# Optimization experiments

Measured on AMD Instinct MI355X. Metric: run time of the kernel, lower is better.

Reference implementation:

```python
import jax, jax.numpy as jnp
import numpy as np

H = 1024   # hidden_size
E = 6      # num_experts
LS = 4     # sparse (MoE) layers
LD = 4     # dense layers
CAP = 4    # expert capacity: max(min(1, int(1*1.25/6)), MIN_EXPERT_CAPACITY=4)
LOSS_COEF = 0.01
SECOND_THRESHOLD = 0.2
EPS = 1e-9


def _bn(x, g, b):
    # BatchNorm1d, training-style batch statistics (biased variance), eps=1e-5
    mu = x.mean(0)
    var = ((x - mu) ** 2).mean(0)
    return g * (x - mu) * jax.lax.rsqrt(var + 1e-5) + b


def _top2_gating(x, wg, key):
    # x: (b, n=1, d) -> dispatch/combine (b, n, e, cap), scalar aux loss
    dt = x.dtype
    raw = jax.nn.softmax(jnp.einsum('bnd,de->bne', x, wg), axis=-1)
    idx1 = jnp.argmax(raw, -1)
    m1 = jax.nn.one_hot(idx1, E, dtype=dt)
    g1 = jnp.sum(raw * m1, -1)
    wo1 = raw * (1.0 - m1)
    idx2 = jnp.argmax(wo1, -1)
    m2 = jax.nn.one_hot(idx2, E, dtype=dt)
    g2 = jnp.sum(wo1 * m2, -1)
    den = g1 + g2 + EPS
    g1, g2 = g1 / den, g2 / den
    # load-balancing loss
    loss = jnp.mean(raw.mean(-2) * m1.mean(-2)) * (E * E)
    # 'random' second-expert policy
    probs = jax.random.uniform(key, g2.shape, dtype=dt)
    m2 = m2 * (probs < (g2 / SECOND_THRESHOLD)).astype(dt)[..., None]
    # positions in capacity buffer (exclusive cumsum over token dim)
    p1 = (jnp.cumsum(m1, axis=1) - m1) * m1
    m1 = m1 * (p1 < CAP).astype(dt)
    m1_cnt = m1.sum(axis=1, keepdims=True)
    m1_flat = m1.sum(-1)
    p1 = p1.sum(-1)
    g1 = g1 * m1_flat
    p2 = ((jnp.cumsum(m2, axis=1) - m2) + m1_cnt) * m2
    m2 = m2 * (p2 < CAP).astype(dt)
    m2_flat = m2.sum(-1)
    p2 = p2.sum(-1)
    g2 = g2 * m2_flat
    ohc1 = jax.nn.one_hot(p1.astype(jnp.int32), CAP, dtype=dt)
    ohc2 = jax.nn.one_hot(p2.astype(jnp.int32), CAP, dtype=dt)
    combine = ((g1 * m1_flat)[..., None, None]
               * jax.nn.one_hot(idx1, E, dtype=dt)[..., None] * ohc1[..., None, :]
               + (g2 * m2_flat)[..., None, None]
               * jax.nn.one_hot(idx2, E, dtype=dt)[..., None] * ohc2[..., None, :])
    dispatch = (combine != 0).astype(dt)
    return dispatch, combine, loss


def _moe_layer(x, W, b, g, be, wg, w1, key):
    x = x @ W + b                      # Linear
    raw = x
    x3 = x[:, None, :]                 # SqueezeLayer: (b, 1, d)
    dispatch, combine, loss = _top2_gating(x3, wg, key)
    ei = jnp.einsum('bnd,bnec->ebcd', x3, dispatch)   # (E, b, CAP, d)
    e, bb, c, d = ei.shape
    eo = jax.nn.relu(jnp.einsum('end,edh->enh', ei.reshape(e, bb * c, d), w1))
    out = jnp.einsum('ebcd,bnec->bnd', eo.reshape(e, bb, c, d), combine)[:, 0, :]
    x = raw + out                      # residual
    x = jax.nn.relu(_bn(x, g, be))     # dropout inactive (eval)
    return x, LOSS_COEF * loss


def setup_inputs() -> dict:
    key = jax.random.key(0)
    ks = jax.random.split(key, 8)
    B, IN, OUT = 2048, 2048, 256
    sc = lambda f: 1.0 / np.sqrt(f)
    f32 = jnp.float32
    return {
        'x': jax.random.normal(ks[0], (B, IN), f32),
        'in_W': jax.random.normal(ks[1], (IN, H), f32) * sc(IN),
        'in_b': jnp.zeros((H,), f32),
        'in_g': jnp.ones((H,), f32),
        'in_be': jnp.zeros((H,), f32),
        'sp_W': jax.random.normal(ks[2], (LS, H, H), f32) * sc(H),
        'sp_b': jnp.zeros((LS, H), f32),
        'sp_g': jnp.ones((LS, H), f32),
        'sp_be': jnp.zeros((LS, H), f32),
        'sp_gate': jax.random.normal(ks[3], (LS, H, E), f32) * sc(H),
        'sp_w1': jax.random.normal(ks[4], (LS, E, H, H), f32) * sc(H),
        'dn_W': jax.random.normal(ks[5], (LD, H, H), f32) * sc(H),
        'dn_b': jnp.zeros((LD, H), f32),
        'dn_g': jnp.ones((LD, H), f32),
        'dn_be': jnp.zeros((LD, H), f32),
        'out_W': jax.random.normal(ks[6], (H, OUT), f32) * sc(H),
        'out_b': jnp.zeros((OUT,), f32),
    }


def reference(x, in_W, in_b, in_g, in_be, sp_W, sp_b, sp_g, sp_be, sp_gate, sp_w1,
              dn_W, dn_b, dn_g, dn_be, out_W, out_b):
    h = jax.nn.relu(_bn(x @ in_W + in_b, in_g, in_be))  # input layer (dropout eval)
    loss = jnp.zeros((), h.dtype)
    base = jax.random.key(42)
    for i in range(LS):
        h, l = _moe_layer(h, sp_W[i], sp_b[i], sp_g[i], sp_be[i],
                          sp_gate[i], sp_w1[i], jax.random.fold_in(base, i))
        loss = loss + l
    for i in range(LD):
        h = jax.nn.relu(_bn(h @ dn_W[i] + dn_b[i], dn_g[i], dn_be[i]))
    return h @ out_W + out_b, loss
```

## Files before the change

kernel.cpp:

```cpp
#include <hip/hip_runtime.h>

typedef unsigned int uint;
typedef unsigned short ushort;
typedef short bf16x8 __attribute__((ext_vector_type(8)));
typedef ushort ushort4v __attribute__((ext_vector_type(4)));
typedef float f32x4 __attribute__((ext_vector_type(4)));

#define HD 1024
#define BT 2048
#define NEXP 6
#define MAXR 4096
#define GT 16

typedef __attribute__((address_space(1))) void as1_void;
typedef __attribute__((address_space(3))) void as3_void;
#define ASYNC16(g, l) \
  __builtin_amdgcn_global_load_lds((as1_void*)(const void*)(g), (as3_void*)(void*)(l), 16, 0, 0)

__device__ static inline ushort f32_to_bf16(float f) {
  uint u = __float_as_uint(f);
  u = (u + 0x7fffu + ((u >> 16) & 1u)) >> 16;
  return (ushort)u;
}
__device__ static inline float bf16_to_f32(ushort h) {
  return __uint_as_float(((uint)h) << 16);
}
__device__ static inline void split2(float f, ushort* hi, ushort* lo) {
  ushort h = f32_to_bf16(f);
  *hi = h;
  *lo = f32_to_bf16(f - bf16_to_f32(h));
}

__host__ __device__ static inline unsigned rotl32(unsigned v, int n) {
  return (v << n) | (v >> (32 - n));
}
__host__ __device__ static inline void tf2x32(unsigned k0, unsigned k1,
                                              unsigned x0, unsigned x1,
                                              unsigned* o0, unsigned* o1) {
  unsigned ks0 = k0, ks1 = k1, ks2 = k0 ^ k1 ^ 0x1BD11BDAu;
  x0 += ks0; x1 += ks1;
  const int ra[4] = {13, 15, 26, 6};
  const int rb[4] = {17, 29, 16, 24};
  #pragma unroll
  for (int r = 0; r < 4; ++r) { x0 += x1; x1 = rotl32(x1, ra[r]); x1 ^= x0; }
  x0 += ks1; x1 += ks2 + 1u;
  #pragma unroll
  for (int r = 0; r < 4; ++r) { x0 += x1; x1 = rotl32(x1, rb[r]); x1 ^= x0; }
  x0 += ks2; x1 += ks0 + 2u;
  #pragma unroll
  for (int r = 0; r < 4; ++r) { x0 += x1; x1 = rotl32(x1, ra[r]); x1 ^= x0; }
  x0 += ks0; x1 += ks1 + 3u;
  #pragma unroll
  for (int r = 0; r < 4; ++r) { x0 += x1; x1 = rotl32(x1, rb[r]); x1 ^= x0; }
  x0 += ks1; x1 += ks2 + 4u;
  #pragma unroll
  for (int r = 0; r < 4; ++r) { x0 += x1; x1 = rotl32(x1, ra[r]); x1 ^= x0; }
  x0 += ks2; x1 += ks0 + 5u;
  *o0 = x0; *o1 = x1;
}

__global__ void init_ws_k(int* cnt, float* loss) {
  int t = threadIdx.x;
  if (t < 32) cnt[t] = 0;
  if (t == 32) loss[0] = 0.0f;
}

__global__ __launch_bounds__(256) void transpose_split_k(
    const float* __restrict__ W, ushort* __restrict__ Th, ushort* __restrict__ Tl,
    int K, int N) {
  size_t boff = (size_t)blockIdx.z * K * N;
  W += boff; Th += boff; Tl += boff;
  __shared__ float T[32][33];
  int n0 = blockIdx.x * 32, k0 = blockIdx.y * 32;
  int tid = threadIdx.x;
  int r = tid >> 3, c4 = (tid & 7) * 4;
  float4 v = *(const float4*)&W[(size_t)(k0 + r) * N + n0 + c4];
  T[c4 + 0][r] = v.x; T[c4 + 1][r] = v.y; T[c4 + 2][r] = v.z; T[c4 + 3][r] = v.w;
  __syncthreads();
  ushort4v hh, ll;
  #pragma unroll
  for (int j = 0; j < 4; ++j) {
    float f = T[r][c4 + j];
    ushort h, l; split2(f, &h, &l);
    hh[j] = h; ll[j] = l;
  }
  size_t o = (size_t)(n0 + r) * K + k0 + c4;
  *(ushort4v*)&Th[o] = hh;
  *(ushort4v*)&Tl[o] = ll;
}

__global__ __launch_bounds__(256) void split_plain_k(
    const float* __restrict__ X, ushort* __restrict__ Xh, ushort* __restrict__ Xl) {
  size_t i = ((size_t)blockIdx.x * 256 + threadIdx.x) * 4;
  float4 v = *(const float4*)&X[i];
  ushort4v hh, ll;
  float f[4] = {v.x, v.y, v.z, v.w};
  #pragma unroll
  for (int j = 0; j < 4; ++j) { ushort h, l; split2(f[j], &h, &l); hh[j] = h; ll[j] = l; }
  *(ushort4v*)&Xh[i] = hh;
  *(ushort4v*)&Xl[i] = ll;
}

template <int MODE>
__global__ __launch_bounds__(512, 4) void gemm_mfma_k(
    const ushort* __restrict__ Ah, const ushort* __restrict__ Al,
    const ushort* __restrict__ Bh, const ushort* __restrict__ Bl,
    float* __restrict__ P,
    const int* __restrict__ cnt, const int* __restrict__ list,
    int N, int K, int ksteps) {
  int bz = blockIdx.z;
  int row0 = blockIdx.y * 128, col0 = blockIdx.x * 128;
  int nrows = 0, kbase = 0;
  if (MODE == 2) {
    size_t wo = (size_t)bz * N * K;
    Bh += wo; Bl += wo;
    nrows = cnt[bz];
    list += bz * MAXR;
    if (row0 >= nrows) return;
  } else {
    P += (size_t)bz * BT * N;
    kbase = bz * ksteps * 32;
  }
  __shared__ ushort sAh[2][4096], sAl[2][4096], sBh[2][4096], sBl[2][4096];
  int tid = threadIdx.x;
  int lane = tid & 63, w = tid >> 6;
  int wm = (w & 3) * 32, wn = (w >> 2) * 64;

  const ushort *pAh, *pAl, *pBh, *pBl;
  {
    int ci = tid;
    int r = ci >> 2;
    int cl = (ci & 3) ^ ((r ^ (r >> 2)) & 3);
    int ra = row0 + r;
    if (MODE == 2) ra = (ra < nrows) ? (list[ra] & (BT - 1)) : 0;
    size_t ao = (size_t)ra * K + kbase + cl * 8;
    size_t bo = (size_t)(col0 + r) * K + kbase + cl * 8;
    pAh = Ah + ao; pAl = Al + ao;
    pBh = Bh + bo; pBl = Bl + bo;
  }
  int lb = w * 512;

  int fr = lane & 15, cq = lane >> 4;
  int offA[2], offB[4];
  #pragma unroll
  for (int i = 0; i < 2; ++i) {
    int rA = wm + i * 16 + fr;
    offA[i] = rA * 32 + (cq ^ ((rA ^ (rA >> 2)) & 3)) * 8;
  }
  #pragma unroll
  for (int i = 0; i < 4; ++i) {
    int rB = wn + i * 16 + fr;
    offB[i] = rB * 32 + (cq ^ ((rB ^ (rB >> 2)) & 3)) * 8;
  }

  f32x4 acc[2][4] = {};

#define STAGE(buf, ko)                    \
  do {                                    \
    ASYNC16(pAh + (ko), sAh[buf] + lb);   \
    ASYNC16(pAl + (ko), sAl[buf] + lb);   \
    ASYNC16(pBh + (ko), sBh[buf] + lb);   \
    ASYNC16(pBl + (ko), sBl[buf] + lb);   \
  } while (0)

  STAGE(0, 0);
  __syncthreads();

  int cur = 0;
  for (int ks = 0; ks < ksteps; ++ks) {
    if (ks + 1 < ksteps) STAGE(cur ^ 1, (ks + 1) * 32);

    bf16x8 ah[2], al[2], bh[4], bl[4];
    #pragma unroll
    for (int i = 0; i < 2; ++i) {
      ah[i] = *(const bf16x8*)&sAh[cur][offA[i]];
      al[i] = *(const bf16x8*)&sAl[cur][offA[i]];
    }
    #pragma unroll
    for (int i = 0; i < 4; ++i) {
      bh[i] = *(const bf16x8*)&sBh[cur][offB[i]];
      bl[i] = *(const bf16x8*)&sBl[cur][offB[i]];
    }
    __builtin_amdgcn_s_setprio(1);
    #pragma unroll
    for (int mi = 0; mi < 2; ++mi)
      #pragma unroll
      for (int ni = 0; ni < 4; ++ni) {
        acc[mi][ni] = __builtin_amdgcn_mfma_f32_16x16x32_bf16(ah[mi], bh[ni], acc[mi][ni], 0, 0, 0);
        acc[mi][ni] = __builtin_amdgcn_mfma_f32_16x16x32_bf16(ah[mi], bl[ni], acc[mi][ni], 0, 0, 0);
        acc[mi][ni] = __builtin_amdgcn_mfma_f32_16x16x32_bf16(al[mi], bh[ni], acc[mi][ni], 0, 0, 0);
      }
    __builtin_amdgcn_s_setprio(0);
    __syncthreads();
    cur ^= 1;
  }
#undef STAGE

  if (MODE == 2) {
    #pragma unroll
    for (int mi = 0; mi < 2; ++mi) {
      int rb = row0 + wm + mi * 16 + cq * 4;
      #pragma unroll
      for (int r = 0; r < 4; ++r) {
        int row = rb + r;
        if (row < nrows) {
          size_t dro = (size_t)list[row] * N;
          #pragma unroll
          for (int ni = 0; ni < 4; ++ni)
            P[dro + col0 + wn + ni * 16 + fr] = fmaxf(acc[mi][ni][r], 0.0f);
        }
      }
    }
  } else {
    #pragma unroll
    for (int mi = 0; mi < 2; ++mi) {
      int rb = row0 + wm + mi * 16 + cq * 4;
      #pragma unroll
      for (int r = 0; r < 4; ++r) {
        size_t ro = (size_t)(rb + r) * N;
        #pragma unroll
        for (int ni = 0; ni < 4; ++ni)
          P[ro + col0 + wn + ni * 16 + fr] = acc[mi][ni][r];
      }
    }
  }
}

template <int NS>
__global__ __launch_bounds__(256) void reduce_dense_k(
    const float* __restrict__ P, const float* __restrict__ bias,
    float* __restrict__ xl, float* __restrict__ psum) {
  int c = blockIdx.x * 256 + threadIdx.x;
  int r0 = blockIdx.y * 64;
  float bv = bias[c];
  float s = 0.0f;
  for (int r = r0; r < r0 + 64; ++r) {
    float v = bv;
    #pragma unroll
    for (int j = 0; j < NS; ++j) v += P[(size_t)j * BT * HD + (size_t)r * HD + c];
    xl[(size_t)r * HD + c] = v;
    s += v;
  }
  psum[blockIdx.y * HD + c] = s;
}

template <int NS>
__global__ __launch_bounds__(256) void reduce_split_k(
    const float* __restrict__ P, const float* __restrict__ bias,
    float* __restrict__ xl, ushort* __restrict__ Xh, ushort* __restrict__ Xl2) {
  int c = blockIdx.x * 256 + threadIdx.x;
  int r0 = blockIdx.y * 64;
  float bv = bias[c];
  for (int r = r0; r < r0 + 64; ++r) {
    float v = bv;
    #pragma unroll
    for (int j = 0; j < NS; ++j) v += P[(size_t)j * BT * HD + (size_t)r * HD + c];
    xl[(size_t)r * HD + c] = v;
    ushort h, l; split2(v, &h, &l);
    Xh[(size_t)r * HD + c] = h;
    Xl2[(size_t)r * HD + c] = l;
  }
}

__global__ __launch_bounds__(256) void reduce_out_k(
    const float* __restrict__ P, const float* __restrict__ bias,
    float* __restrict__ out) {
  int c = threadIdx.x;
  int r0 = blockIdx.y * 64;
  float bv = bias[c];
  for (int r = r0; r < r0 + 64; ++r) {
    float v = bv;
    #pragma unroll
    for (int j = 0; j < 8; ++j) v += P[(size_t)j * BT * 256 + (size_t)r * 256 + c];
    out[(size_t)r * 256 + c] = v;
  }
}

__global__ __launch_bounds__(256) void gating_k(
    const float* __restrict__ xl, const float* __restrict__ wg,
    int* __restrict__ cnt, int* __restrict__ toklist,
    float* __restrict__ g1o, float* __restrict__ g2o,
    float* __restrict__ loss, unsigned key0, unsigned key1) {
  int tid = threadIdx.x;
  int lane = tid & 63, wv = tid >> 6;
  int q = lane >> 4, ql = lane & 15;
  int t = wv * 4 + q;
  int b = blockIdx.x * GT + t;

  const float* row = xl + (size_t)b * HD;
  float p[NEXP] = {0, 0, 0, 0, 0, 0};
  for (int d = ql; d < HD; d += 16) {
    float xv = row[d];
    const float* w = wg + (size_t)d * NEXP;
    #pragma unroll
    for (int e = 0; e < NEXP; ++e) p[e] += xv * w[e];
  }
  #pragma unroll
  for (int off = 8; off > 0; off >>= 1)
    #pragma unroll
    for (int e = 0; e < NEXP; ++e) p[e] += __shfl_xor(p[e], off);

  __shared__ int   li1[GT], li2[GT];
  __shared__ float lg1[GT], lg2[GT], lgg1[GT];
  __shared__ int   base_s[NEXP];

  if (ql == 0) {
    float mx = p[0];
    #pragma unroll
    for (int e = 1; e < NEXP; ++e) mx = fmaxf(mx, p[e]);
    float ex[NEXP], s = 0.0f;
    #pragma unroll
    for (int e = 0; e < NEXP; ++e) { ex[e] = expf(p[e] - mx); s += ex[e]; }
    float raw[NEXP];
    #pragma unroll
    for (int e = 0; e < NEXP; ++e) raw[e] = ex[e] / s;
    int i1 = 0; float gg1 = raw[0];
    #pragma unroll
    for (int e = 1; e < NEXP; ++e) if (raw[e] > gg1) { gg1 = raw[e]; i1 = e; }
    int i2 = -1; float gg2 = -1.0f;
    #pragma unroll
    for (int e = 0; e < NEXP; ++e) {
      float v = (e == i1) ? 0.0f : raw[e];
      if (v > gg2) { gg2 = v; i2 = e; }
    }
    float den = gg1 + gg2 + 1e-9f;
    float g1n = gg1 / den;
    float g2n = gg2 / den;
    unsigned o0, o1;
    tf2x32(key0, key1, 0u, (unsigned)b, &o0, &o1);
    unsigned bits = o0 ^ o1;
    float prob = __uint_as_float((bits >> 9) | 0x3f800000u) - 1.0f;
    int keep = prob < (g2n / 0.2f);
    li1[t] = i1;
    li2[t] = keep ? i2 : -1;
    lg1[t] = g1n;
    lg2[t] = keep ? g2n : 0.0f;
    lgg1[t] = gg1;
  }
  __syncthreads();

  if (tid < NEXP) {
    int c = 0;
    for (int j = 0; j < GT; ++j) c += (li1[j] == tid) + (li2[j] == tid);
    base_s[tid] = (c > 0) ? atomicAdd(&cnt[tid], c) : 0;
  }
  if (tid == 64) {
    float s = 0.0f;
    for (int j = 0; j < GT; ++j) s += lgg1[j];
    atomicAdd(loss, s);
  }
  __syncthreads();

  if (tid < GT) {
    int tt = tid;
    int i1 = li1[tt], i2 = li2[tt];
    int bb = blockIdx.x * GT + tt;
    g1o[bb] = lg1[tt];
    g2o[bb] = lg2[tt];
    int o1 = 0, o2 = 0;
    for (int j = 0; j < tt; ++j) {
      o1 += (li1[j] == i1) + (li2[j] == i1);
      o2 += (li1[j] == i2) + (li2[j] == i2);
    }
    toklist[i1 * MAXR + base_s[i1] + o1] = bb;
    if (i2 >= 0) toklist[i2 * MAXR + base_s[i2] + o2] = BT + bb;
  }
}

__global__ __launch_bounds__(256) void combine_sum_k(
    const float* __restrict__ xl, const float* __restrict__ eo,
    const float* __restrict__ g1o, const float* __restrict__ g2o,
    float* __restrict__ y, float* __restrict__ psum) {
  int c = blockIdx.x * 256 + threadIdx.x;
  int r0 = blockIdx.y * 64;
  float s = 0.0f;
  for (int r = r0; r < r0 + 64; ++r) {
    float v = xl[(size_t)r * HD + c];
    float w1g = g1o[r];
    v += w1g * eo[(size_t)r * HD + c];
    float w2g = g2o[r];
    if (w2g != 0.0f) v += w2g * eo[(size_t)(r + BT) * HD + c];
    y[(size_t)r * HD + c] = v;
    s += v;
  }
  psum[blockIdx.y * HD + c] = s;
}

__global__ __launch_bounds__(256) void var_partial_k(
    const float* __restrict__ src, const float* __restrict__ psum,
    float* __restrict__ psumsq) {
  int c = blockIdx.x * 256 + threadIdx.x;
  float s = 0.0f;
  #pragma unroll
  for (int i = 0; i < 32; ++i) s += psum[i * HD + c];
  float mu = s * (1.0f / 2048.0f);
  int r0 = blockIdx.y * 64;
  float ss = 0.0f;
  for (int r = r0; r < r0 + 64; ++r) {
    float d = src[(size_t)r * HD + c] - mu;
    ss += d * d;
  }
  psumsq[blockIdx.y * HD + c] = ss;
}

__global__ __launch_bounds__(256) void bn_split_k(
    const float* __restrict__ src, const float* __restrict__ psum,
    const float* __restrict__ psumsq, const float* __restrict__ gamma,
    const float* __restrict__ beta, ushort* __restrict__ Hh,
    ushort* __restrict__ Hl) {
  int c = blockIdx.x * 256 + threadIdx.x;
  float s = 0.0f, ss = 0.0f;
  #pragma unroll
  for (int i = 0; i < 32; ++i) { s += psum[i * HD + c]; ss += psumsq[i * HD + c]; }
  float mu = s * (1.0f / 2048.0f);
  float var = ss * (1.0f / 2048.0f);
  float inv = 1.0f / sqrtf(var + 1e-5f);
  float ga = gamma[c], be = beta[c];
  int r0 = blockIdx.y * 64;
  for (int r = r0; r < r0 + 64; ++r) {
    float v = src[(size_t)r * HD + c];
    float o = fmaxf(ga * (v - mu) * inv + be, 0.0f);
    ushort h, l; split2(o, &h, &l);
    Hh[(size_t)r * HD + c] = h;
    Hl[(size_t)r * HD + c] = l;
  }
}

__global__ void finalize_loss_k(const float* __restrict__ loss, float* __restrict__ out) {
  if (threadIdx.x == 0) out[BT * 256] = loss[0] * (0.01f * 36.0f / 12288.0f);
}

extern "C" void kernel_launch(void* const* d_in, const int* in_sizes, int n_in,
                              void* d_out, int out_size, void* d_ws, size_t ws_size,
                              hipStream_t stream) {
  const float* x     = (const float*)d_in[0];
  const float* in_W  = (const float*)d_in[1];
  const float* in_b  = (const float*)d_in[2];
  const float* in_g  = (const float*)d_in[3];
  const float* in_be = (const float*)d_in[4];
  const float* sp_W  = (const float*)d_in[5];
  const float* sp_b  = (const float*)d_in[6];
  const float* sp_g  = (const float*)d_in[7];
  const float* sp_be = (const float*)d_in[8];
  const float* sp_gate = (const float*)d_in[9];
  const float* sp_w1 = (const float*)d_in[10];
  const float* dn_W  = (const float*)d_in[11];
  const float* dn_b  = (const float*)d_in[12];
  const float* dn_g  = (const float*)d_in[13];
  const float* dn_be = (const float*)d_in[14];
  const float* out_W = (const float*)d_in[15];
  const float* out_b = (const float*)d_in[16];
  float* out = (float*)d_out;

  char* base = (char*)d_ws;
  size_t off = 0;
  auto alloc = [&](size_t bytes) { void* p = base + off; off = (off + bytes + 255) & ~(size_t)255; return p; };
  float*  xl     = (float*)alloc((size_t)BT * HD * 4);
  float*  P      = (float*)alloc((size_t)4 * BT * HD * 4);
  float*  eo     = P;
  float*  y      = P + (size_t)4 * 1024 * 1024;
  float*  psum   = (float*)alloc(32 * HD * 4);
  float*  psumsq = (float*)alloc(32 * HD * 4);
  float*  g1o    = (float*)alloc(BT * 4);
  float*  g2o    = (float*)alloc(BT * 4);
  float*  loss   = (float*)alloc(256);
  int*    cnt    = (int*)alloc(256);
  int*    toklist= (int*)alloc(NEXP * MAXR * 4);
  ushort* Hh     = (ushort*)alloc((size_t)BT * HD * 2);
  ushort* Hl     = (ushort*)alloc((size_t)BT * HD * 2);
  ushort* XLh    = (ushort*)alloc((size_t)BT * HD * 2);
  ushort* XLl    = (ushort*)alloc((size_t)BT * HD * 2);
  ushort* inWTh  = (ushort*)alloc((size_t)2048 * HD * 2);
  ushort* inWTl  = (ushort*)alloc((size_t)2048 * HD * 2);
  ushort* spWTh  = (ushort*)alloc((size_t)4 * HD * HD * 2);
  ushort* spWTl  = (ushort*)alloc((size_t)4 * HD * HD * 2);
  ushort* dnWTh  = (ushort*)alloc((size_t)4 * HD * HD * 2);
  ushort* dnWTl  = (ushort*)alloc((size_t)4 * HD * HD * 2);
  ushort* outWTh = (ushort*)alloc((size_t)HD * 256 * 2);
  ushort* outWTl = (ushort*)alloc((size_t)HD * 256 * 2);
  ushort* w1Th   = (ushort*)alloc((size_t)24 * HD * HD * 2);
  ushort* w1Tl   = (ushort*)alloc((size_t)24 * HD * HD * 2);
  ushort* Xh     = w1Th;
  ushort* Xl     = w1Th + (size_t)BT * 2048;

  unsigned lk0[4], lk1[4];
  for (int i = 0; i < 4; ++i) tf2x32(0u, 42u, 0u, (unsigned)i, &lk0[i], &lk1[i]);

  dim3 blk(256);
  dim3 gblk(512);
  init_ws_k<<<1, 64, 0, stream>>>(cnt, loss);

  transpose_split_k<<<dim3(32, 64, 1), blk, 0, stream>>>(in_W, inWTh, inWTl, 2048, HD);
  transpose_split_k<<<dim3(32, 32, 4), blk, 0, stream>>>(sp_W, spWTh, spWTl, HD, HD);
  transpose_split_k<<<dim3(32, 32, 4), blk, 0, stream>>>(dn_W, dnWTh, dnWTl, HD, HD);
  transpose_split_k<<<dim3(8, 32, 1), blk, 0, stream>>>(out_W, outWTh, outWTl, HD, 256);
  split_plain_k<<<(BT * 2048) / 1024, blk, 0, stream>>>(x, Xh, Xl);

  gemm_mfma_k<0><<<dim3(8, 16, 4), gblk, 0, stream>>>(Xh, Xl, inWTh, inWTl, P,
                                                      nullptr, nullptr, HD, 2048, 16);
  reduce_dense_k<4><<<dim3(4, 32), blk, 0, stream>>>(P, in_b, xl, psum);
  transpose_split_k<<<dim3(32, 32, 24), blk, 0, stream>>>(sp_w1, w1Th, w1Tl, HD, HD);
  var_partial_k<<<dim3(4, 32), blk, 0, stream>>>(xl, psum, psumsq);
  bn_split_k<<<dim3(4, 32), blk, 0, stream>>>(xl, psum, psumsq, in_g, in_be, Hh, Hl);

  for (int i = 0; i < 4; ++i) {
    gemm_mfma_k<0><<<dim3(8, 16, 4), gblk, 0, stream>>>(Hh, Hl, spWTh + (size_t)i * HD * HD,
                                                        spWTl + (size_t)i * HD * HD, P,
                                                        nullptr, nullptr, HD, HD, 8);
    reduce_split_k<4><<<dim3(4, 32), blk, 0, stream>>>(P, sp_b + i * HD, xl, XLh, XLl);
    gating_k<<<BT / GT, blk, 0, stream>>>(xl, sp_gate + (size_t)i * HD * NEXP,
                                          cnt + i * 8, toklist, g1o, g2o, loss, lk0[i], lk1[i]);
    gemm_mfma_k<2><<<dim3(8, 32, NEXP), gblk, 0, stream>>>(XLh, XLl,
                                                           w1Th + (size_t)i * NEXP * HD * HD,
                                                           w1Tl + (size_t)i * NEXP * HD * HD,
                                                           eo, cnt + i * 8, toklist, HD, HD, 32);
    combine_sum_k<<<dim3(4, 32), blk, 0, stream>>>(xl, eo, g1o, g2o, y, psum);
    var_partial_k<<<dim3(4, 32), blk, 0, stream>>>(y, psum, psumsq);
    bn_split_k<<<dim3(4, 32), blk, 0, stream>>>(y, psum, psumsq, sp_g + i * HD,
                                                sp_be + i * HD, Hh, Hl);
  }

  for (int i = 0; i < 4; ++i) {
    gemm_mfma_k<0><<<dim3(8, 16, 4), gblk, 0, stream>>>(Hh, Hl, dnWTh + (size_t)i * HD * HD,
                                                        dnWTl + (size_t)i * HD * HD, P,
                                                        nullptr, nullptr, HD, HD, 8);
    reduce_dense_k<4><<<dim3(4, 32), blk, 0, stream>>>(P, dn_b + i * HD, xl, psum);
    var_partial_k<<<dim3(4, 32), blk, 0, stream>>>(xl, psum, psumsq);
    bn_split_k<<<dim3(4, 32), blk, 0, stream>>>(xl, psum, psumsq, dn_g + i * HD,
                                                dn_be + i * HD, Hh, Hl);
  }

  gemm_mfma_k<0><<<dim3(2, 16, 8), gblk, 0, stream>>>(Hh, Hl, outWTh, outWTl, P,
                                                      nullptr, nullptr, 256, HD, 4);
  reduce_out_k<<<dim3(1, 32), blk, 0, stream>>>(P, out_b, out);
  finalize_loss_k<<<1, 64, 0, stream>>>(loss, out);
}
```

Baseline: 1.147 ms.

## Narrow GEMM tiles to 128x64 and widen reduction grids with separate BN fold kernels

```diff
diff --git a/kernel.cpp b/kernel.cpp
--- a/kernel.cpp
+++ b/kernel.cpp
@@ -11,6 +11,8 @@
 #define NEXP 6
 #define MAXR 4096
 #define GT 16
+#define NG 128
+#define RG 16
 
 typedef __attribute__((address_space(1))) void as1_void;
 typedef __attribute__((address_space(3))) void as3_void;
@@ -102,14 +104,14 @@
 }
 
 template <int MODE>
-__global__ __launch_bounds__(512, 4) void gemm_mfma_k(
+__global__ __launch_bounds__(512, 6) void gemm_mfma_k(
     const ushort* __restrict__ Ah, const ushort* __restrict__ Al,
     const ushort* __restrict__ Bh, const ushort* __restrict__ Bl,
     float* __restrict__ P,
     const int* __restrict__ cnt, const int* __restrict__ list,
     int N, int K, int ksteps) {
   int bz = blockIdx.z;
-  int row0 = blockIdx.y * 128, col0 = blockIdx.x * 128;
+  int row0 = blockIdx.y * 128, col0 = blockIdx.x * 64;
   int nrows = 0, kbase = 0;
   if (MODE == 2) {
     size_t wo = (size_t)bz * N * K;
@@ -121,46 +123,49 @@
     P += (size_t)bz * BT * N;
     kbase = bz * ksteps * 32;
   }
-  __shared__ ushort sAh[2][4096], sAl[2][4096], sBh[2][4096], sBl[2][4096];
+  __shared__ ushort sAh[2][4096], sAl[2][4096], sBh[2][2048], sBl[2][2048];
   int tid = threadIdx.x;
   int lane = tid & 63, w = tid >> 6;
-  int wm = (w & 3) * 32, wn = (w >> 2) * 64;
-
-  const ushort *pAh, *pAl, *pBh, *pBl;
+  int wm = (w & 3) * 32;
+  int wn = (w >> 2) * 32;
+
+  const ushort *pAh, *pAl, *pBh = Bh, *pBl = Bl;
   {
-    int ci = tid;
-    int r = ci >> 2;
-    int cl = (ci & 3) ^ ((r ^ (r >> 2)) & 3);
+    int r = tid >> 2;
+    int cl = (tid & 3) ^ ((r ^ (r >> 2)) & 3);
     int ra = row0 + r;
     if (MODE == 2) ra = (ra < nrows) ? (list[ra] & (BT - 1)) : 0;
     size_t ao = (size_t)ra * K + kbase + cl * 8;
+    pAh = Ah + ao; pAl = Al + ao;
+  }
+  if (tid < 256) {
+    int r = tid >> 2;
+    int cl = (tid & 3) ^ ((r ^ (r >> 2)) & 3);
     size_t bo = (size_t)(col0 + r) * K + kbase + cl * 8;
-    pAh = Ah + ao; pAl = Al + ao;
     pBh = Bh + bo; pBl = Bl + bo;
   }
   int lb = w * 512;
 
   int fr = lane & 15, cq = lane >> 4;
-  int offA[2], offB[4];
+  int offA[2], offB[2];
   #pragma unroll
   for (int i = 0; i < 2; ++i) {
     int rA = wm + i * 16 + fr;
     offA[i] = rA * 32 + (cq ^ ((rA ^ (rA >> 2)) & 3)) * 8;
-  }
-  #pragma unroll
-  for (int i = 0; i < 4; ++i) {
     int rB = wn + i * 16 + fr;
     offB[i] = rB * 32 + (cq ^ ((rB ^ (rB >> 2)) & 3)) * 8;
   }
 
-  f32x4 acc[2][4] = {};
-
-#define STAGE(buf, ko)                    \
-  do {                                    \
-    ASYNC16(pAh + (ko), sAh[buf] + lb);   \
-    ASYNC16(pAl + (ko), sAl[buf] + lb);   \
-    ASYNC16(pBh + (ko), sBh[buf] + lb);   \
-    ASYNC16(pBl + (ko), sBl[buf] + lb);   \
+  f32x4 acc[2][2] = {};
+
+#define STAGE(buf, ko)                       \
+  do {                                       \
+    ASYNC16(pAh + (ko), sAh[buf] + lb);      \
+    ASYNC16(pAl + (ko), sAl[buf] + lb);      \
+    if (w < 4) {                             \
+      ASYNC16(pBh + (ko), sBh[buf] + lb);    \
+      ASYNC16(pBl + (ko), sBl[buf] + lb);    \
+    }                                        \
   } while (0)
 
   STAGE(0, 0);
@@ -170,14 +175,11 @@
   for (int ks = 0; ks < ksteps; ++ks) {
     if (ks + 1 < ksteps) STAGE(cur ^ 1, (ks + 1) * 32);
 
-    bf16x8 ah[2], al[2], bh[4], bl[4];
+    bf16x8 ah[2], al[2], bh[2], bl[2];
     #pragma unroll
     for (int i = 0; i < 2; ++i) {
       ah[i] = *(const bf16x8*)&sAh[cur][offA[i]];
       al[i] = *(const bf16x8*)&sAl[cur][offA[i]];
-    }
-    #pragma unroll
-    for (int i = 0; i < 4; ++i) {
       bh[i] = *(const bf16x8*)&sBh[cur][offB[i]];
       bl[i] = *(const bf16x8*)&sBl[cur][offB[i]];
     }
@@ -185,7 +187,7 @@
     #pragma unroll
     for (int mi = 0; mi < 2; ++mi)
       #pragma unroll
-      for (int ni = 0; ni < 4; ++ni) {
+      for (int ni = 0; ni < 2; ++ni) {
         acc[mi][ni] = __builtin_amdgcn_mfma_f32_16x16x32_bf16(ah[mi], bh[ni], acc[mi][ni], 0, 0, 0);
         acc[mi][ni] = __builtin_amdgcn_mfma_f32_16x16x32_bf16(ah[mi], bl[ni], acc[mi][ni], 0, 0, 0);
         acc[mi][ni] = __builtin_amdgcn_mfma_f32_16x16x32_bf16(al[mi], bh[ni], acc[mi][ni], 0, 0, 0);
@@ -206,7 +208,7 @@
         if (row < nrows) {
           size_t dro = (size_t)list[row] * N;
           #pragma unroll
-          for (int ni = 0; ni < 4; ++ni)
+          for (int ni = 0; ni < 2; ++ni)
             P[dro + col0 + wn + ni * 16 + fr] = fmaxf(acc[mi][ni][r], 0.0f);
         }
       }
@@ -219,7 +221,7 @@
       for (int r = 0; r < 4; ++r) {
         size_t ro = (size_t)(rb + r) * N;
         #pragma unroll
-        for (int ni = 0; ni < 4; ++ni)
+        for (int ni = 0; ni < 2; ++ni)
           P[ro + col0 + wn + ni * 16 + fr] = acc[mi][ni][r];
       }
     }
@@ -231,10 +233,10 @@
     const float* __restrict__ P, const float* __restrict__ bias,
     float* __restrict__ xl, float* __restrict__ psum) {
   int c = blockIdx.x * 256 + threadIdx.x;
-  int r0 = blockIdx.y * 64;
+  int r0 = blockIdx.y * RG;
   float bv = bias[c];
   float s = 0.0f;
-  for (int r = r0; r < r0 + 64; ++r) {
+  for (int r = r0; r < r0 + RG; ++r) {
     float v = bv;
     #pragma unroll
     for (int j = 0; j < NS; ++j) v += P[(size_t)j * BT * HD + (size_t)r * HD + c];
@@ -249,9 +251,9 @@
     const float* __restrict__ P, const float* __restrict__ bias,
     float* __restrict__ xl, ushort* __restrict__ Xh, ushort* __restrict__ Xl2) {
   int c = blockIdx.x * 256 + threadIdx.x;
-  int r0 = blockIdx.y * 64;
+  int r0 = blockIdx.y * RG;
   float bv = bias[c];
-  for (int r = r0; r < r0 + 64; ++r) {
+  for (int r = r0; r < r0 + RG; ++r) {
     float v = bv;
     #pragma unroll
     for (int j = 0; j < NS; ++j) v += P[(size_t)j * BT * HD + (size_t)r * HD + c];
@@ -266,9 +268,9 @@
     const float* __restrict__ P, const float* __restrict__ bias,
     float* __restrict__ out) {
   int c = threadIdx.x;
-  int r0 = blockIdx.y * 64;
+  int r0 = blockIdx.y * RG;
   float bv = bias[c];
-  for (int r = r0; r < r0 + 64; ++r) {
+  for (int r = r0; r < r0 + RG; ++r) {
     float v = bv;
     #pragma unroll
     for (int j = 0; j < 8; ++j) v += P[(size_t)j * BT * 256 + (size_t)r * 256 + c];
@@ -372,9 +374,9 @@
     const float* __restrict__ g1o, const float* __restrict__ g2o,
     float* __restrict__ y, float* __restrict__ psum) {
   int c = blockIdx.x * 256 + threadIdx.x;
-  int r0 = blockIdx.y * 64;
+  int r0 = blockIdx.y * RG;
   float s = 0.0f;
-  for (int r = r0; r < r0 + 64; ++r) {
+  for (int r = r0; r < r0 + RG; ++r) {
     float v = xl[(size_t)r * HD + c];
     float w1g = g1o[r];
     v += w1g * eo[(size_t)r * HD + c];
@@ -386,17 +388,31 @@
   psum[blockIdx.y * HD + c] = s;
 }
 
+__global__ __launch_bounds__(256) void fold_mu_k(
+    const float* __restrict__ psum, float* __restrict__ mu) {
+  int c = blockIdx.x * 256 + threadIdx.x;
+  float s = 0.0f;
+  for (int i = 0; i < NG; ++i) s += psum[i * HD + c];
+  mu[c] = s * (1.0f / 2048.0f);
+}
+
+__global__ __launch_bounds__(256) void fold_inv_k(
+    const float* __restrict__ psumsq, float* __restrict__ inv) {
+  int c = blockIdx.x * 256 + threadIdx.x;
+  float ss = 0.0f;
+  for (int i = 0; i < NG; ++i) ss += psumsq[i * HD + c];
+  float var = ss * (1.0f / 2048.0f);
+  inv[c] = 1.0f / sqrtf(var + 1e-5f);
+}
+
 __global__ __launch_bounds__(256) void var_partial_k(
-    const float* __restrict__ src, const float* __restrict__ psum,
+    const float* __restrict__ src, const float* __restrict__ mu_,
     float* __restrict__ psumsq) {
   int c = blockIdx.x * 256 + threadIdx.x;
-  float s = 0.0f;
-  #pragma unroll
-  for (int i = 0; i < 32; ++i) s += psum[i * HD + c];
-  float mu = s * (1.0f / 2048.0f);
-  int r0 = blockIdx.y * 64;
+  float mu = mu_[c];
+  int r0 = blockIdx.y * RG;
   float ss = 0.0f;
-  for (int r = r0; r < r0 + 64; ++r) {
+  for (int r = r0; r < r0 + RG; ++r) {
     float d = src[(size_t)r * HD + c] - mu;
     ss += d * d;
   }
@@ -404,20 +420,16 @@
 }
 
 __global__ __launch_bounds__(256) void bn_split_k(
-    const float* __restrict__ src, const float* __restrict__ psum,
-    const float* __restrict__ psumsq, const float* __restrict__ gamma,
+    const float* __restrict__ src, const float* __restrict__ mu_,
+    const float* __restrict__ inv_, const float* __restrict__ gamma,
     const float* __restrict__ beta, ushort* __restrict__ Hh,
     ushort* __restrict__ Hl) {
   int c = blockIdx.x * 256 + threadIdx.x;
-  float s = 0.0f, ss = 0.0f;
-  #pragma unroll
-  for (int i = 0; i < 32; ++i) { s += psum[i * HD + c]; ss += psumsq[i * HD + c]; }
-  float mu = s * (1.0f / 2048.0f);
-  float var = ss * (1.0f / 2048.0f);
-  float inv = 1.0f / sqrtf(var + 1e-5f);
+  float mu = mu_[c];
+  float inv = inv_[c];
   float ga = gamma[c], be = beta[c];
-  int r0 = blockIdx.y * 64;
-  for (int r = r0; r < r0 + 64; ++r) {
+  int r0 = blockIdx.y * RG;
+  for (int r = r0; r < r0 + RG; ++r) {
     float v = src[(size_t)r * HD + c];
     float o = fmaxf(ga * (v - mu) * inv + be, 0.0f);
     ushort h, l; split2(o, &h, &l);
@@ -459,8 +471,10 @@
   float*  P      = (float*)alloc((size_t)4 * BT * HD * 4);
   float*  eo     = P;
   float*  y      = P + (size_t)4 * 1024 * 1024;
-  float*  psum   = (float*)alloc(32 * HD * 4);
-  float*  psumsq = (float*)alloc(32 * HD * 4);
+  float*  psum   = (float*)alloc(NG * HD * 4);
+  float*  psumsq = (float*)alloc(NG * HD * 4);
+  float*  muv    = (float*)alloc(HD * 4);
+  float*  invv   = (float*)alloc(HD * 4);
   float*  g1o    = (float*)alloc(BT * 4);
   float*  g2o    = (float*)alloc(BT * 4);
   float*  loss   = (float*)alloc(256);
@@ -496,42 +510,48 @@
   transpose_split_k<<<dim3(8, 32, 1), blk, 0, stream>>>(out_W, outWTh, outWTl, HD, 256);
   split_plain_k<<<(BT * 2048) / 1024, blk, 0, stream>>>(x, Xh, Xl);
 
-  gemm_mfma_k<0><<<dim3(8, 16, 4), gblk, 0, stream>>>(Xh, Xl, inWTh, inWTl, P,
-                                                      nullptr, nullptr, HD, 2048, 16);
-  reduce_dense_k<4><<<dim3(4, 32), blk, 0, stream>>>(P, in_b, xl, psum);
+  gemm_mfma_k<0><<<dim3(16, 16, 4), gblk, 0, stream>>>(Xh, Xl, inWTh, inWTl, P,
+                                                       nullptr, nullptr, HD, 2048, 16);
+  reduce_dense_k<4><<<dim3(4, NG), blk, 0, stream>>>(P, in_b, xl, psum);
   transpose_split_k<<<dim3(32, 32, 24), blk, 0, stream>>>(sp_w1, w1Th, w1Tl, HD, HD);
-  var_partial_k<<<dim3(4, 32), blk, 0, stream>>>(xl, psum, psumsq);
-  bn_split_k<<<dim3(4, 32), blk, 0, stream>>>(xl, psum, psumsq, in_g, in_be, Hh, Hl);
+  fold_mu_k<<<4, blk, 0, stream>>>(psum, muv);
+  var_partial_k<<<dim3(4, NG), blk, 0, stream>>>(xl, muv, psumsq);
+  fold_inv_k<<<4, blk, 0, stream>>>(psumsq, invv);
+  bn_split_k<<<dim3(4, NG), blk, 0, stream>>>(xl, muv, invv, in_g, in_be, Hh, Hl);
 
   for (int i = 0; i < 4; ++i) {
-    gemm_mfma_k<0><<<dim3(8, 16, 4), gblk, 0, stream>>>(Hh, Hl, spWTh + (size_t)i * HD * HD,
-                                                        spWTl + (size_t)i * HD * HD, P,
-                                                        nullptr, nullptr, HD, HD, 8);
-    reduce_split_k<4><<<dim3(4, 32), blk, 0, stream>>>(P, sp_b + i * HD, xl, XLh, XLl);
+    gemm_mfma_k<0><<<dim3(16, 16, 4), gblk, 0, stream>>>(Hh, Hl, spWTh + (size_t)i * HD * HD,
+                                                         spWTl + (size_t)i * HD * HD, P,
+                                                         nullptr, nullptr, HD, HD, 8);
+    reduce_split_k<4><<<dim3(4, NG), blk, 0, stream>>>(P, sp_b + i * HD, xl, XLh, XLl);
     gating_k<<<BT / GT, blk, 0, stream>>>(xl, sp_gate + (size_t)i * HD * NEXP,
                                           cnt + i * 8, toklist, g1o, g2o, loss, lk0[i], lk1[i]);
-    gemm_mfma_k<2><<<dim3(8, 32, NEXP), gblk, 0, stream>>>(XLh, XLl,
-                                                           w1Th + (size_t)i * NEXP * HD * HD,
-                                                           w1Tl + (size_t)i * NEXP * HD * HD,
-                                                           eo, cnt + i * 8, toklist, HD, HD, 32);
-    combine_sum_k<<<dim3(4, 32), blk, 0, stream>>>(xl, eo, g1o, g2o, y, psum);
-    var_partial_k<<<dim3(4, 32), blk, 0, stream>>>(y, psum, psumsq);
-    bn_split_k<<<dim3(4, 32), blk, 0, stream>>>(y, psum, psumsq, sp_g + i * HD,
+    gemm_mfma_k<2><<<dim3(16, 32, NEXP), gblk, 0, stream>>>(XLh, XLl,
+                                                            w1Th + (size_t)i * NEXP * HD * HD,
+                                                            w1Tl + (size_t)i * NEXP * HD * HD,
+                                                            eo, cnt + i * 8, toklist, HD, HD, 32);
+    combine_sum_k<<<dim3(4, NG), blk, 0, stream>>>(xl, eo, g1o, g2o, y, psum);
+    fold_mu_k<<<4, blk, 0, stream>>>(psum, muv);
+    var_partial_k<<<dim3(4, NG), blk, 0, stream>>>(y, muv, psumsq);
+    fold_inv_k<<<4, blk, 0, stream>>>(psumsq, invv);
+    bn_split_k<<<dim3(4, NG), blk, 0, stream>>>(y, muv, invv, sp_g + i * HD,
                                                 sp_be + i * HD, Hh, Hl);
   }
 
   for (int i = 0; i < 4; ++i) {
-    gemm_mfma_k<0><<<dim3(8, 16, 4), gblk, 0, stream>>>(Hh, Hl, dnWTh + (size_t)i * HD * HD,
-                                                        dnWTl + (size_t)i * HD * HD, P,
-                                                        nullptr, nullptr, HD, HD, 8);
-    reduce_dense_k<4><<<dim3(4, 32), blk, 0, stream>>>(P, dn_b + i * HD, xl, psum);
-    var_partial_k<<<dim3(4, 32), blk, 0, stream>>>(xl, psum, psumsq);
-    bn_split_k<<<dim3(4, 32), blk, 0, stream>>>(xl, psum, psumsq, dn_g + i * HD,
+    gemm_mfma_k<0><<<dim3(16, 16, 4), gblk, 0, stream>>>(Hh, Hl, dnWTh + (size_t)i * HD * HD,
+                                                         dnWTl + (size_t)i * HD * HD, P,
+                                                         nullptr, nullptr, HD, HD, 8);
+    reduce_dense_k<4><<<dim3(4, NG), blk, 0, stream>>>(P, dn_b + i * HD, xl, psum);
+    fold_mu_k<<<4, blk, 0, stream>>>(psum, muv);
+    var_partial_k<<<dim3(4, NG), blk, 0, stream>>>(xl, muv, psumsq);
+    fold_inv_k<<<4, blk, 0, stream>>>(psumsq, invv);
+    bn_split_k<<<dim3(4, NG), blk, 0, stream>>>(xl, muv, invv, dn_g + i * HD,
                                                 dn_be + i * HD, Hh, Hl);
   }
 
-  gemm_mfma_k<0><<<dim3(2, 16, 8), gblk, 0, stream>>>(Hh, Hl, outWTh, outWTl, P,
+  gemm_mfma_k<0><<<dim3(4, 16, 8), gblk, 0, stream>>>(Hh, Hl, outWTh, outWTl, P,
                                                       nullptr, nullptr, 256, HD, 4);
-  reduce_out_k<<<dim3(1, 32), blk, 0, stream>>>(P, out_b, out);
+  reduce_out_k<<<dim3(1, NG), blk, 0, stream>>>(P, out_b, out);
   finalize_loss_k<<<1, 64, 0, stream>>>(loss, out);
 }
```

Result: faster. 1.098 ms (-4.3%).
